# Kernel tuning notes

Hardware: AMD Instinct MI355X
Metric: run time of the kernel (lower is better)

Reference implementation:

```python
import jax, jax.numpy as jnp
import numpy as np

B, S, H = 2, 2048, 768
NH, HD = 12, 64  # num heads, head dim


def setup_inputs() -> dict:
    key = jax.random.key(0)
    ks = jax.random.split(key, 9)
    std = 0.02
    def dense(k):
        return jax.random.normal(k, (H, H), dtype=jnp.float32) * std
    return {
        "hidden_states": jax.random.normal(ks[0], (B, S, H), dtype=jnp.float32),
        "attention_mask": jnp.ones((B, S), dtype=jnp.int32),
        "Wq": dense(ks[1]), "bq": jnp.zeros((H,), jnp.float32),
        "Wk": dense(ks[2]), "bk": jnp.zeros((H,), jnp.float32),
        "Wv": dense(ks[3]), "bv": jnp.zeros((H,), jnp.float32),
        "Wo": dense(ks[4]), "bo": jnp.zeros((H,), jnp.float32),
    }


def reference(hidden_states, attention_mask, Wq, bq, Wk, bk, Wv, bv, Wo, bo):
    # QKV projections -> [B, NH, S, HD]
    def split_heads(x):
        return x.reshape(B, S, NH, HD).transpose(0, 2, 1, 3)
    q = split_heads(hidden_states @ Wq + bq)
    k = split_heads(hidden_states @ Wk + bk)
    v = split_heads(hidden_states @ Wv + bv)
    # scaled dot-product scores [B, NH, S, S]
    scores = jnp.einsum('bhqd,bhkd->bhqk', q, k) / jnp.sqrt(jnp.float32(HD))
    adder = (1.0 - attention_mask.astype(jnp.float32)) * -10000.0
    scores = scores + adder[:, None, None, :]
    probs = jax.nn.softmax(scores, axis=-1)
    # dropout is identity at inference
    ctx = jnp.einsum('bhqk,bhkd->bhqd', probs, v)
    ctx = ctx.transpose(0, 2, 1, 3).reshape(B, S, H)
    return ctx @ Wo + bo
```

## Files before the change

### kernel.cpp

```cpp
#include <hip/hip_runtime.h>
#include <hip/hip_bf16.h>

#define DI __device__ __forceinline__

using bf16x8 = __attribute__((ext_vector_type(8))) short;
using f32x4  = __attribute__((ext_vector_type(4))) float;
using f32x16 = __attribute__((ext_vector_type(16))) float;
using u16    = unsigned short;
using u16x4  = __attribute__((ext_vector_type(4))) unsigned short;

constexpr int Bc = 2, Sc = 2048, Hc = 768, NHc = 12, HDc = 64;
constexpr int Mc = Bc * Sc;
constexpr float L2E = 1.4426950408889634f;

DI u16 f2bf(float f) {
  union { float f; unsigned u; } c; c.f = f;
  unsigned u = c.u;
  return (u16)((u + 0x7fffu + ((u >> 16) & 1u)) >> 16);
}

DI unsigned f2bf2(float a, float b) {
  float2 t; t.x = a; t.y = b;
  __hip_bfloat162 h = __float22bfloat162_rn(t);
  union { __hip_bfloat162 h; unsigned u; } c; c.h = h;
  return c.u;
}

DI void gload_lds16(const void* g, void* l) {
  __builtin_amdgcn_global_load_lds(
      (__attribute__((address_space(1))) void*)(g),
      (__attribute__((address_space(3))) void*)(l), 16, 0, 0);
}


__global__ void cvt_bf16(const float* __restrict__ x, u16* __restrict__ y, int n4,
                         const int* __restrict__ maskg, u16* __restrict__ mones) {
  int i = blockIdx.x * 256 + threadIdx.x;
  if (i >= n4) return;
  float4 v = reinterpret_cast<const float4*>(x)[i];
  u16x4 o;
  o[0] = f2bf(v.x); o[1] = f2bf(v.y); o[2] = f2bf(v.z); o[3] = f2bf(v.w);
  reinterpret_cast<u16x4*>(y)[i] = o;
  if (i < Bc * Sc / 4) {
    int4 mv = reinterpret_cast<const int4*>(maskg)[i];
    u16x4 m;
    m[0] = f2bf((float)mv.x); m[1] = f2bf((float)mv.y);
    m[2] = f2bf((float)mv.z); m[3] = f2bf((float)mv.w);
    reinterpret_cast<u16x4*>(mones)[i] = m;
  }
}

__global__ void wtrans(const float* __restrict__ Wq, const float* __restrict__ Wk,
                       const float* __restrict__ Wv, const float* __restrict__ Wo,
                       u16* __restrict__ Tq, u16* __restrict__ Tk,
                       u16* __restrict__ Tv, u16* __restrict__ To) {
  __shared__ float tile[32][33];
  const float* W; u16* T;
  switch (blockIdx.z) {
    case 0:  W = Wq; T = Tq; break;
    case 1:  W = Wk; T = Tk; break;
    case 2:  W = Wv; T = Tv; break;
    default: W = Wo; T = To; break;
  }
  int tx = threadIdx.x, ty = threadIdx.y;
  int n0 = blockIdx.x * 32, k0 = blockIdx.y * 32;
#pragma unroll
  for (int j = 0; j < 4; ++j) tile[ty + j * 8][tx] = W[(k0 + ty + j * 8) * Hc + n0 + tx];
  __syncthreads();
#pragma unroll
  for (int j = 0; j < 4; ++j) T[(n0 + ty + j * 8) * Hc + k0 + tx] = f2bf(tile[tx][ty + j * 8]);
}


DI void gemm_core(const u16* __restrict__ Ag, const u16* __restrict__ Btg,
                  u16* Asm, u16* Bsm, int m0, int n0,
                  int tid, int lane, int wr, int wc, f32x4 acc[4][4]) {
  const int lo = lane & 15, hi = lane >> 4;
  const int r1 = tid >> 2, c1 = tid & 3;
  for (int kt = 0; kt < Hc / 32; ++kt) {
    const int k0 = kt * 32;
    {
      int row = r1, cg = c1 ^ ((row >> 1) & 3);
      gload_lds16(Ag  + (size_t)(row + m0) * Hc + k0 + cg * 8, Asm + tid * 8);
      gload_lds16(Btg + (size_t)(row + n0) * Hc + k0 + cg * 8, Bsm + tid * 8);
      row = r1 + 64; cg = c1 ^ ((row >> 1) & 3);
      gload_lds16(Ag  + (size_t)(row + m0) * Hc + k0 + cg * 8, Asm + (tid + 256) * 8);
      gload_lds16(Btg + (size_t)(row + n0) * Hc + k0 + cg * 8, Bsm + (tid + 256) * 8);
    }
    __syncthreads();
    bf16x8 af[4], bf[4];
#pragma unroll
    for (int m = 0; m < 4; ++m) {
      int rowa = wr * 64 + m * 16 + lo;
      af[m] = *reinterpret_cast<const bf16x8*>(Asm + rowa * 32 + ((hi ^ ((rowa >> 1) & 3)) * 8));
      int rowb = wc * 64 + m * 16 + lo;
      bf[m] = *reinterpret_cast<const bf16x8*>(Bsm + rowb * 32 + ((hi ^ ((rowb >> 1) & 3)) * 8));
    }
#pragma unroll
    for (int m = 0; m < 4; ++m)
#pragma unroll
      for (int n = 0; n < 4; ++n)
        acc[m][n] = __builtin_amdgcn_mfma_f32_16x16x32_bf16(af[m], bf[n], acc[m][n], 0, 0, 0);
    __syncthreads();
  }
}


__launch_bounds__(256)
__global__ void qkv_gemm(const u16* __restrict__ Xb,
                         const u16* __restrict__ Wtq, const u16* __restrict__ Wtk,
                         const u16* __restrict__ Wtv,
                         const float* __restrict__ bq, const float* __restrict__ bk,
                         const float* __restrict__ bv, const int* __restrict__ maskg,
                         u16* __restrict__ Qo, u16* __restrict__ Ko, u16* __restrict__ Vto) {
  __shared__ __attribute__((aligned(16))) u16 Asm[128 * 32];
  __shared__ __attribute__((aligned(16))) u16 Bsm[128 * 32];
  const int tid = threadIdx.x, lane = tid & 63, w = tid >> 6;
  const int wr = w >> 1, wc = w & 1;
  const int m0 = blockIdx.x * 128, n0 = blockIdx.y * 128;
  const int z = blockIdx.z;
  const u16* Bt = (z == 0) ? Wtq : ((z == 1) ? Wtk : Wtv);
  const float* bias = (z == 0) ? bq : ((z == 1) ? bk : bv);
  f32x4 acc[4][4] = {};
  gemm_core(Xb, Bt, Asm, Bsm, m0, n0, tid, lane, wr, wc, acc);
  const int lo = lane & 15, hi = lane >> 4;
  const float scl = (z == 0) ? 0.125f * L2E : 1.0f;
#pragma unroll
  for (int m = 0; m < 4; ++m)
#pragma unroll
    for (int n = 0; n < 4; ++n)
#pragma unroll
      for (int r = 0; r < 4; ++r) {
        int gm = m0 + wr * 64 + m * 16 + hi * 4 + r;
        int gn = n0 + wc * 64 + n * 16 + lo;
        float v = (acc[m][n][r] + bias[gn]) * scl;
        int b = gm >> 11, s = gm & 2047, h = gn >> 6, d = gn & 63;
        if (z == 2) {
          v *= (float)maskg[b * Sc + s];
          Vto[((b * NHc + h) * HDc + d) * Sc + s] = f2bf(v);
        } else {
          int idx = (((b * NHc + h) * Sc) + s) * HDc + d;
          if (z == 0) Qo[idx] = f2bf(v); else Ko[idx] = f2bf(v);
        }
      }
}


__launch_bounds__(256)
__global__ void out_gemm(const u16* __restrict__ Ctx, const u16* __restrict__ Wto,
                         const float* __restrict__ bo, float* __restrict__ out) {
  __shared__ __attribute__((aligned(16))) u16 Asm[128 * 32];
  __shared__ __attribute__((aligned(16))) u16 Bsm[128 * 32];
  const int tid = threadIdx.x, lane = tid & 63, w = tid >> 6;
  const int wr = w >> 1, wc = w & 1;
  const int m0 = blockIdx.x * 128, n0 = blockIdx.y * 128;
  f32x4 acc[4][4] = {};
  gemm_core(Ctx, Wto, Asm, Bsm, m0, n0, tid, lane, wr, wc, acc);
  const int lo = lane & 15, hi = lane >> 4;
#pragma unroll
  for (int m = 0; m < 4; ++m)
#pragma unroll
    for (int n = 0; n < 4; ++n)
#pragma unroll
      for (int r = 0; r < 4; ++r) {
        int gm = m0 + wr * 64 + m * 16 + hi * 4 + r;
        int gn = n0 + wc * 64 + n * 16 + lo;
        out[(size_t)gm * Hc + gn] = acc[m][n][r] + bo[gn];
      }
}


DI bf16x8 lds_rd(const u16* base, int row, int c8) {
  return *reinterpret_cast<const bf16x8*>(base + row * 64 + ((c8 ^ (row & 7)) << 3));
}

DI bf16x8 ldV(const u16* Vs, int row, int c4, int hi2) {
  union { u16x4 h[2]; bf16x8 v; } u;
  const u16* rbase = Vs + row * 64;
  int sw = (row & 7) << 3;
  u.h[0] = *reinterpret_cast<const u16x4*>(rbase + (((c4 * 16) ) ^ sw) + hi2 * 4);
  u.h[1] = *reinterpret_cast<const u16x4*>(rbase + (((c4 * 16) + 8) ^ sw) + hi2 * 4);
  return u.v;
}

DI bf16x8 ldM(const u16* Mo, int base, int c4, int hi2) {
  union { u16x4 h[2]; bf16x8 v; } u;
  u.h[0] = *reinterpret_cast<const u16x4*>(Mo + base + c4 * 16 + hi2 * 4);
  u.h[1] = *reinterpret_cast<const u16x4*>(Mo + base + c4 * 16 + 8 + hi2 * 4);
  return u.v;
}

DI float vmax16(const f32x16& v) {
  float a0 = fmaxf(v[0], v[8]),  a1 = fmaxf(v[1], v[9]);
  float a2 = fmaxf(v[2], v[10]), a3 = fmaxf(v[3], v[11]);
  float a4 = fmaxf(v[4], v[12]), a5 = fmaxf(v[5], v[13]);
  float a6 = fmaxf(v[6], v[14]), a7 = fmaxf(v[7], v[15]);
  float b0 = fmaxf(a0, a4), b1 = fmaxf(a1, a5);
  float b2 = fmaxf(a2, a6), b3 = fmaxf(a3, a7);
  return fmaxf(fmaxf(b0, b1), fmaxf(b2, b3));
}

DI bf16x8 pkfrag0(const f32x16& p) {
  union { unsigned u[4]; bf16x8 v; } a;
  a.u[0] = f2bf2(p[0], p[1]); a.u[1] = f2bf2(p[2], p[3]);
  a.u[2] = f2bf2(p[4], p[5]); a.u[3] = f2bf2(p[6], p[7]);
  return a.v;
}
DI bf16x8 pkfrag1(const f32x16& p) {
  union { unsigned u[4]; bf16x8 v; } a;
  a.u[0] = f2bf2(p[8], p[9]);   a.u[1] = f2bf2(p[10], p[11]);
  a.u[2] = f2bf2(p[12], p[13]); a.u[3] = f2bf2(p[14], p[15]);
  return a.v;
}

__launch_bounds__(128)
__global__ void attn(const u16* __restrict__ Qg, const u16* __restrict__ Kg,
                     const u16* __restrict__ Vtg, const u16* __restrict__ monesG,
                     u16* __restrict__ ctxg) {
  __shared__ __attribute__((aligned(16))) u16 Ksm[3][64 * 64];
  __shared__ __attribute__((aligned(16))) u16 Vsm[3][64 * 64];
  __shared__ __attribute__((aligned(16))) u16 Mo[Sc];

  const int tid = threadIdx.x, lane = tid & 63, w = tid >> 6;
  const int l31 = lane & 31, hi2 = lane >> 5;

  const int id = blockIdx.x;
  const int xcd = id & 7, sub = id >> 3;
  const int head = xcd * 3 + (sub >> 5);
  const int q0 = (sub & 31) * 64;
  const int b = head / NHc, h = head % NHc;

  const u16* Qh = Qg + (size_t)head * Sc * HDc;
  const u16* Kh = Kg + (size_t)head * Sc * HDc;
  const u16* Vh = Vtg + (size_t)head * HDc * Sc;

#pragma unroll
  for (int j = 0; j < 2; ++j) {
    int ch = tid + j * 128;
    gload_lds16(monesG + (size_t)b * Sc + ch * 8, Mo + ch * 8);
  }

  const int qglob = q0 + w * 32 + l31;
  bf16x8 qf[4];
#pragma unroll
  for (int c = 0; c < 4; ++c)
    qf[c] = *reinterpret_cast<const bf16x8*>(Qh + (size_t)qglob * HDc + c * 16 + hi2 * 8);

  __syncthreads();

  u16 *K0 = &Ksm[0][0], *K1 = &Ksm[1][0], *K2 = &Ksm[2][0];
  u16 *V0 = &Vsm[0][0], *V1 = &Vsm[1][0], *V2 = &Vsm[2][0];

  auto stage = [&](u16* Kd, u16* Vd, int kv0) {
#pragma unroll
    for (int j = 0; j < 4; ++j) {
      int ch = tid + j * 128;
      int row = ch >> 3, cg = (ch & 7) ^ (row & 7);
      gload_lds16(Kh + (size_t)(kv0 + row) * HDc + cg * 8, Kd + ch * 8);
    }
#pragma unroll
    for (int j = 0; j < 4; ++j) {
      int ch = tid + j * 128;
      int row = ch >> 3, cg = (ch & 7) ^ (row & 7);
      gload_lds16(Vh + (size_t)row * Sc + kv0 + cg * 8, Vd + ch * 8);
    }
  };

  stage(K0, V0, 0);
  stage(K1, V1, 64);

  f32x16 oacc0 = {}, oacc1 = {}, lacc = {};
  float mrow = -1e30f;

  constexpr int NT = Sc / 64;
  for (int t = 0; t < NT; ++t) {
    __builtin_amdgcn_sched_barrier(0);
    __builtin_amdgcn_s_barrier();
    __builtin_amdgcn_sched_barrier(0);
    if (t + 2 < NT) {
      stage(K2, V2, (t + 2) * 64);
      asm volatile("s_waitcnt vmcnt(16)" ::: "memory");
    } else if (t + 2 == NT) {
      asm volatile("s_waitcnt vmcnt(8)" ::: "memory");
    } else {
      asm volatile("s_waitcnt vmcnt(0)" ::: "memory");
    }
    __builtin_amdgcn_sched_barrier(0);
    __builtin_amdgcn_s_barrier();
    __builtin_amdgcn_sched_barrier(0);

    const u16* Ks = K0;
    const u16* Vs = V0;

    f32x16 s0 = {}, s1 = {};
#pragma unroll
    for (int c = 0; c < 4; ++c) {
      bf16x8 kf0 = lds_rd(Ks, l31, 2 * c + hi2);
      bf16x8 kf1 = lds_rd(Ks, 32 + l31, 2 * c + hi2);
      s0 = __builtin_amdgcn_mfma_f32_32x32x16_bf16(kf0, qf[c], s0, 0, 0, 0);
      s1 = __builtin_amdgcn_mfma_f32_32x32x16_bf16(kf1, qf[c], s1, 0, 0, 0);
    }

    float pmax = fmaxf(vmax16(s0), vmax16(s1));
    pmax = fmaxf(pmax, __shfl_xor(pmax, 32, 64));
    float nm = fmaxf(mrow, pmax);
    float sc = exp2f(mrow - nm);
    mrow = nm;
#pragma unroll
    for (int rr = 0; rr < 16; ++rr) {
      int qi = (rr & 3) + 8 * (rr >> 2) + 4 * hi2;
      float sb = __shfl(sc, qi, 64);
      oacc0[rr] *= sb; oacc1[rr] *= sb; lacc[rr] *= sb;
    }
#pragma unroll
    for (int j = 0; j < 16; ++j) s0[j] = exp2f(s0[j] - mrow);
#pragma unroll
    for (int j = 0; j < 16; ++j) s1[j] = exp2f(s1[j] - mrow);

    bf16x8 paf[4];
    paf[0] = pkfrag0(s0);
    paf[1] = pkfrag1(s0);
    paf[2] = pkfrag0(s1);
    paf[3] = pkfrag1(s1);

#pragma unroll
    for (int c4 = 0; c4 < 4; ++c4) {
      bf16x8 mo = ldM(Mo, t * 64, c4, hi2);
      lacc = __builtin_amdgcn_mfma_f32_32x32x16_bf16(paf[c4], mo, lacc, 0, 0, 0);
      bf16x8 vf0 = ldV(Vs, l31, c4, hi2);
      bf16x8 vf1 = ldV(Vs, 32 + l31, c4, hi2);
      oacc0 = __builtin_amdgcn_mfma_f32_32x32x16_bf16(paf[c4], vf0, oacc0, 0, 0, 0);
      oacc1 = __builtin_amdgcn_mfma_f32_32x32x16_bf16(paf[c4], vf1, oacc1, 0, 0, 0);
    }

    u16* tk = K0; K0 = K1; K1 = K2; K2 = tk;
    u16* tv = V0; V0 = V1; V1 = V2; V2 = tv;
  }

#pragma unroll
  for (int rr = 0; rr < 16; ++rr) {
    float inv = 1.0f / lacc[rr];
    int qi = (rr & 3) + 8 * (rr >> 2) + 4 * hi2;
    int s = q0 + w * 32 + qi;
    size_t base = (size_t)(b * Sc + s) * Hc + h * HDc;
    ctxg[base + l31]      = f2bf(oacc0[rr] * inv);
    ctxg[base + 32 + l31] = f2bf(oacc1[rr] * inv);
  }
}


extern "C" void kernel_launch(void* const* d_in, const int* in_sizes, int n_in,
                              void* d_out, int out_size, void* d_ws, size_t ws_size,
                              hipStream_t stream) {
  const float* hs  = (const float*)d_in[0];
  const int* mask  = (const int*)d_in[1];
  const float* Wq  = (const float*)d_in[2];
  const float* bq  = (const float*)d_in[3];
  const float* Wk  = (const float*)d_in[4];
  const float* bk  = (const float*)d_in[5];
  const float* Wv  = (const float*)d_in[6];
  const float* bv  = (const float*)d_in[7];
  const float* Wo  = (const float*)d_in[8];
  const float* bo  = (const float*)d_in[9];

  char* ws = (char*)d_ws;
  u16* Xb  = (u16*)(ws);
  u16* Wtq = (u16*)(ws + 6291456);
  u16* Wtk = Wtq + 589824;
  u16* Wtv = Wtk + 589824;
  u16* Wto = Wtv + 589824;
  u16* Qb  = (u16*)(ws + 11010048);
  u16* Kb  = Qb + 3145728;
  u16* Vtb = Kb + 3145728;
  u16* Ctx = Vtb + 3145728;
  u16* Mns = Ctx + 3145728;

  cvt_bf16<<<(Mc * Hc / 4 + 255) / 256, 256, 0, stream>>>(hs, Xb, Mc * Hc / 4, mask, Mns);
  wtrans<<<dim3(24, 24, 4), dim3(32, 8), 0, stream>>>(Wq, Wk, Wv, Wo, Wtq, Wtk, Wtv, Wto);
  qkv_gemm<<<dim3(32, 6, 3), 256, 0, stream>>>(Xb, Wtq, Wtk, Wtv, bq, bk, bv, mask, Qb, Kb, Vtb);
  attn<<<768, 128, 0, stream>>>(Qb, Kb, Vtb, Mns, Ctx);
  out_gemm<<<dim3(32, 6), 256, 0, stream>>>(Ctx, Wto, bo, (float*)d_out);
}
```

Before: 156.8 us.

## Permute V and mask layout for 128-bit LDS reads, add lazy rescale and setprio

The V-transpose store and the bf16 mask conversion now permute the sequence index (bits 2 and 3 swapped), so each lane's PV operand fragment is contiguous. That lets the PV loop use one 128-bit swizzled LDS read per fragment instead of two 64-bit reads. The online-softmax rescale of the accumulators is skipped unless the new row max exceeds the running max by more than 8 (log2 units), which saves shuffles and multiplies but can let exponents grow up to 2^8. s_setprio raises wave priority around the MFMA blocks.

```diff
diff --git a/kernel.cpp b/kernel.cpp
--- a/kernel.cpp
+++ b/kernel.cpp
@@ -42,7 +42,10 @@
   o[0] = f2bf(v.x); o[1] = f2bf(v.y); o[2] = f2bf(v.z); o[3] = f2bf(v.w);
   reinterpret_cast<u16x4*>(y)[i] = o;
   if (i < Bc * Sc / 4) {
-    int4 mv = reinterpret_cast<const int4*>(maskg)[i];
+    int j = i & 3;
+    int js = ((j & 1) << 1) | ((j >> 1) & 1);
+    int isrc = (i & ~3) | js;
+    int4 mv = reinterpret_cast<const int4*>(maskg)[isrc];
     u16x4 m;
     m[0] = f2bf((float)mv.x); m[1] = f2bf((float)mv.y);
     m[2] = f2bf((float)mv.z); m[3] = f2bf((float)mv.w);
@@ -137,7 +140,8 @@
         int b = gm >> 11, s = gm & 2047, h = gn >> 6, d = gn & 63;
         if (z == 2) {
           v *= (float)maskg[b * Sc + s];
-          Vto[((b * NHc + h) * HDc + d) * Sc + s] = f2bf(v);
+          int sp = (s & ~12) | ((s & 4) << 1) | ((s & 8) >> 1);
+          Vto[((b * NHc + h) * HDc + d) * Sc + sp] = f2bf(v);
         } else {
           int idx = (((b * NHc + h) * Sc) + s) * HDc + d;
           if (z == 0) Qo[idx] = f2bf(v); else Ko[idx] = f2bf(v);
@@ -172,22 +176,6 @@
 
 DI bf16x8 lds_rd(const u16* base, int row, int c8) {
   return *reinterpret_cast<const bf16x8*>(base + row * 64 + ((c8 ^ (row & 7)) << 3));
-}
-
-DI bf16x8 ldV(const u16* Vs, int row, int c4, int hi2) {
-  union { u16x4 h[2]; bf16x8 v; } u;
-  const u16* rbase = Vs + row * 64;
-  int sw = (row & 7) << 3;
-  u.h[0] = *reinterpret_cast<const u16x4*>(rbase + (((c4 * 16) ) ^ sw) + hi2 * 4);
-  u.h[1] = *reinterpret_cast<const u16x4*>(rbase + (((c4 * 16) + 8) ^ sw) + hi2 * 4);
-  return u.v;
-}
-
-DI bf16x8 ldM(const u16* Mo, int base, int c4, int hi2) {
-  union { u16x4 h[2]; bf16x8 v; } u;
-  u.h[0] = *reinterpret_cast<const u16x4*>(Mo + base + c4 * 16 + hi2 * 4);
-  u.h[1] = *reinterpret_cast<const u16x4*>(Mo + base + c4 * 16 + 8 + hi2 * 4);
-  return u.v;
 }
 
 DI float vmax16(const f32x16& v) {
@@ -293,6 +281,7 @@
     const u16* Vs = V0;
 
     f32x16 s0 = {}, s1 = {};
+    __builtin_amdgcn_s_setprio(1);
 #pragma unroll
     for (int c = 0; c < 4; ++c) {
       bf16x8 kf0 = lds_rd(Ks, l31, 2 * c + hi2);
@@ -300,17 +289,20 @@
       s0 = __builtin_amdgcn_mfma_f32_32x32x16_bf16(kf0, qf[c], s0, 0, 0, 0);
       s1 = __builtin_amdgcn_mfma_f32_32x32x16_bf16(kf1, qf[c], s1, 0, 0, 0);
     }
+    __builtin_amdgcn_s_setprio(0);
 
     float pmax = fmaxf(vmax16(s0), vmax16(s1));
     pmax = fmaxf(pmax, __shfl_xor(pmax, 32, 64));
-    float nm = fmaxf(mrow, pmax);
-    float sc = exp2f(mrow - nm);
-    mrow = nm;
-#pragma unroll
-    for (int rr = 0; rr < 16; ++rr) {
-      int qi = (rr & 3) + 8 * (rr >> 2) + 4 * hi2;
-      float sb = __shfl(sc, qi, 64);
-      oacc0[rr] *= sb; oacc1[rr] *= sb; lacc[rr] *= sb;
+    if (!__all(pmax - mrow <= 8.0f)) {
+      float nm = fmaxf(mrow, pmax);
+      float sc = exp2f(mrow - nm);
+      mrow = nm;
+#pragma unroll
+      for (int rr = 0; rr < 16; ++rr) {
+        int qi = (rr & 3) + 8 * (rr >> 2) + 4 * hi2;
+        float sb = __shfl(sc, qi, 64);
+        oacc0[rr] *= sb; oacc1[rr] *= sb; lacc[rr] *= sb;
+      }
     }
 #pragma unroll
     for (int j = 0; j < 16; ++j) s0[j] = exp2f(s0[j] - mrow);
@@ -323,15 +315,17 @@
     paf[2] = pkfrag0(s1);
     paf[3] = pkfrag1(s1);
 
+    __builtin_amdgcn_s_setprio(1);
 #pragma unroll
     for (int c4 = 0; c4 < 4; ++c4) {
-      bf16x8 mo = ldM(Mo, t * 64, c4, hi2);
-      lacc = __builtin_amdgcn_mfma_f32_32x32x16_bf16(paf[c4], mo, lacc, 0, 0, 0);
-      bf16x8 vf0 = ldV(Vs, l31, c4, hi2);
-      bf16x8 vf1 = ldV(Vs, 32 + l31, c4, hi2);
+      bf16x8 mo = *reinterpret_cast<const bf16x8*>(Mo + t * 64 + c4 * 16 + hi2 * 8);
+      bf16x8 vf0 = lds_rd(Vs, l31, 2 * c4 + hi2);
+      bf16x8 vf1 = lds_rd(Vs, 32 + l31, 2 * c4 + hi2);
+      lacc  = __builtin_amdgcn_mfma_f32_32x32x16_bf16(paf[c4], mo, lacc, 0, 0, 0);
       oacc0 = __builtin_amdgcn_mfma_f32_32x32x16_bf16(paf[c4], vf0, oacc0, 0, 0, 0);
       oacc1 = __builtin_amdgcn_mfma_f32_32x32x16_bf16(paf[c4], vf1, oacc1, 0, 0, 0);
     }
+    __builtin_amdgcn_s_setprio(0);
 
     u16* tk = K0; K0 = K1; K1 = K2; K2 = tk;
     u16* tv = V0; V0 = V1; V1 = V2; V2 = tv;
```

Result: faster. 149.1 us (-4.9%).
